# Kernel optimization log

Hardware: AMD Instinct MI355X
Metric: run time of the kernel (lower is better)

## Reference

```python
import jax, jax.numpy as jnp
import numpy as np

B_SI = 4.1491   # neutron scattering length Si (fm)
B_O = 5.803     # neutron scattering length O (fm)
CUTOFF = 3.5    # tetrahedral neighbour cutoff (A)
BIG = 1e6       # masked-distance sentinel (finite to keep grads NaN-free)


def setup_inputs() -> dict:
    key = jax.random.key(0)
    k1, k2 = jax.random.split(key)
    N, L = 4096, 40.0
    positions = jax.random.uniform(k1, (N, 3), dtype=jnp.float32) * L
    cell = (L * jnp.eye(3)).astype(jnp.float32)
    r_bins = (0.05 + 0.05 * jnp.arange(200, dtype=jnp.float32))      # 0.05..10.0 A
    q_bins = jnp.linspace(0.5, 25.0, 500, dtype=jnp.float32)          # A^-1
    species = jax.random.randint(k2, (N,), 0, 3, dtype=jnp.int32)     # 0=Si, 1/2=O
    return {"positions": positions, "cell": cell, "r_bins": r_bins,
            "q_bins": q_bins, "species": species}


def _pair_geometry(positions, cell):
    # Minimum-image displacements under a general periodic cell.
    disp = positions[:, None, :] - positions[None, :, :]        # [N,N,3]
    frac = disp @ jnp.linalg.inv(cell)
    frac = frac - jnp.round(frac)
    disp = frac @ cell
    d2 = jnp.sum(disp * disp, axis=-1)                           # [N,N]
    self_mask = jnp.eye(positions.shape[0], dtype=bool)
    dist = jnp.sqrt(jnp.where(self_mask, 1.0, d2))               # safe sqrt on diag
    return disp, dist, self_mask


def reference(positions, cell, r_bins, q_bins, species):
    N = positions.shape[0]
    nbins = r_bins.shape[0]
    dtype = positions.dtype

    disp, dist, self_mask = _pair_geometry(positions, cell)

    # --- neutron-weighted G(r): differentiable linear (cloud-in-cell) binning ---
    b = jnp.where(species == 0, B_SI, B_O).astype(dtype)         # per-atom scattering length
    w = (b[:, None] * b[None, :]) / (jnp.mean(b) ** 2)           # Faber-Ziman pair weights
    r0, dr = r_bins[0], r_bins[1] - r_bins[0]
    x = (dist - r0) / dr
    i0 = jnp.floor(x).astype(jnp.int32)
    f = x - i0.astype(dtype)
    valid = (~self_mask) & (i0 >= 0) & (i0 < nbins - 1)
    w0 = jnp.where(valid, w * (1.0 - f), 0.0).ravel()
    w1 = jnp.where(valid, w * f, 0.0).ravel()
    i0f = jnp.clip(i0, 0, nbins - 1).ravel()
    hist = (jnp.zeros(nbins, dtype)
            .at[i0f].add(w0)
            .at[jnp.clip(i0f + 1, 0, nbins - 1)].add(w1))
    V = jnp.abs(jnp.linalg.det(cell))
    rho = N / V
    shell = 4.0 * jnp.pi * r_bins ** 2 * dr                       # ideal-gas shell volume
    G_r = hist / (N * rho * shell)                                # [nbins]

    # --- total correlation function T(r) = 4 pi rho r G(r) ---
    T_r = 4.0 * jnp.pi * rho * r_bins * G_r

    # --- structure factor S(Q) = 1 + 4 pi rho int r^2 (G(r)-1) sinc(Qr) dr ---
    qr = q_bins[:, None] * r_bins[None, :]                        # [nQ, nr]
    integrand = (r_bins ** 2) * (G_r - 1.0)
    S_Q = 1.0 + 4.0 * jnp.pi * rho * dr * jnp.sum(
        integrand[None, :] * jnp.sinc(qr / jnp.pi), axis=1)

    # --- tetrahedral order parameter q_tet over Si centres with O neighbours ---
    central = species == 0
    nbr_ok = (species != 0)[None, :] & (~self_mask)
    nd = jnp.where(nbr_ok, dist, BIG)
    negd, idx = jax.lax.top_k(-nd, 4)                             # 4 nearest O per atom
    d4 = -negd                                                    # [N,4]
    u = jnp.take_along_axis(disp, idx[:, :, None], axis=1) / d4[:, :, None]  # unit vecs
    cosang = jnp.einsum('nkd,nld->nkl', u, u)                     # [N,4,4]
    pair_mask = jnp.triu(jnp.ones((4, 4), bool), 1)               # 6 angle pairs
    q_i = 1.0 - (3.0 / 8.0) * jnp.sum(((cosang + 1.0 / 3.0) ** 2) * pair_mask, axis=(1, 2))
    vf = (central & (d4[:, 3] < CUTOFF)).astype(dtype)            # needs 4 nbrs in cutoff
    q_tet = jnp.sum(q_i * vf) / jnp.maximum(jnp.sum(vf), 1.0)

    return G_r, T_r, S_Q, q_tet
```

## Files before the change

kernel.cpp:

```cpp
#include <hip/hip_runtime.h>
#include <climits>
#include <math.h>


#define B_SI_F 4.1491f
#define B_O_F  5.803f
#define CUTOFF_F 3.5f
#define CS2 12.25350025f
#define NCOPIES 16
#define CAP 32

#define WS_HIST 16
#define WS_ACC  3328
#define WS_CNT  4096

__device__ __forceinline__ bool dless(float da, int ia, float db, int ib) {
    return (da < db) || (da == db && ia < ib);
}

struct CellK {
    float ci0, ci1, ci2, ci3, ci4, ci5, ci6, ci7, ci8;
    float c0, c1, c2, c3, c4, c5, c6, c7, c8;
};

__device__ __forceinline__ CellK make_cell(const float* __restrict__ cellm,
                                           bool& diag) {
    CellK K;
    K.c0 = cellm[0]; K.c1 = cellm[1]; K.c2 = cellm[2];
    K.c3 = cellm[3]; K.c4 = cellm[4]; K.c5 = cellm[5];
    K.c6 = cellm[6]; K.c7 = cellm[7]; K.c8 = cellm[8];
    double m0 = K.c0, m1 = K.c1, m2 = K.c2;
    double m3 = K.c3, m4 = K.c4, m5 = K.c5;
    double m6 = K.c6, m7 = K.c7, m8 = K.c8;
    double det = m0*(m4*m8 - m5*m7) - m1*(m3*m8 - m5*m6) + m2*(m3*m7 - m4*m6);
    double rd = 1.0 / det;
    K.ci0 = (float)( (m4*m8 - m5*m7) * rd);
    K.ci1 = (float)(-(m1*m8 - m2*m7) * rd);
    K.ci2 = (float)( (m1*m5 - m2*m4) * rd);
    K.ci3 = (float)(-(m3*m8 - m5*m6) * rd);
    K.ci4 = (float)( (m0*m8 - m2*m6) * rd);
    K.ci5 = (float)(-(m0*m5 - m2*m3) * rd);
    K.ci6 = (float)( (m3*m7 - m4*m6) * rd);
    K.ci7 = (float)(-(m0*m7 - m1*m6) * rd);
    K.ci8 = (float)( (m0*m4 - m1*m3) * rd);
    diag = (K.c1 == 0.0f) && (K.c2 == 0.0f) && (K.c3 == 0.0f) &&
           (K.c5 == 0.0f) && (K.c6 == 0.0f) && (K.c7 == 0.0f);
    return K;
}

template<bool DIAG>
__device__ __forceinline__ void min_image(const CellK& K,
                                          float dx, float dy, float dz,
                                          float& ex, float& ey, float& ez) {
    if (DIAG) {
        float t0 = dx * K.ci0, t1 = dy * K.ci4, t2 = dz * K.ci8;
        t0 -= rintf(t0);  t1 -= rintf(t1);  t2 -= rintf(t2);
        ex = t0 * K.c0;  ey = t1 * K.c4;  ez = t2 * K.c8;
    } else {
        float f0 = dx*K.ci0 + dy*K.ci3 + dz*K.ci6;
        float f1 = dx*K.ci1 + dy*K.ci4 + dz*K.ci7;
        float f2 = dx*K.ci2 + dy*K.ci5 + dz*K.ci8;
        f0 -= rintf(f0);  f1 -= rintf(f1);  f2 -= rintf(f2);
        ex = f0*K.c0 + f1*K.c3 + f2*K.c6;
        ey = f0*K.c1 + f1*K.c4 + f2*K.c7;
        ez = f0*K.c2 + f1*K.c5 + f2*K.c8;
    }
}

template<bool DIAG>
__device__ __forceinline__ void hist_sweep(const CellK& K,
                                           const float4* __restrict__ sj,
                                           const float4* __restrict__ sjc,
                                           int lbase, int jb0,
                                           float fi0, float fi1, float fi2,
                                           float xi, float yi, float zi,
                                           float wi, float inv_dr, float nrb0,
                                           float dmax2, int nbins_m1,
                                           float* shist,
                                           bool iSi, bool iO, bool offdiag, int iidx,
                                           float* __restrict__ cnt,
                                           float4* __restrict__ cand) {
    #pragma unroll 4
    for (int l = 0; l < 32; ++l) {
        const float4 pj = sj[lbase + l];
        float d0 = fi0 - pj.x;  d0 -= rintf(d0);
        float d1 = fi1 - pj.y;  d1 -= rintf(d1);
        float d2 = fi2 - pj.z;  d2 -= rintf(d2);
        float ex, ey, ez;
        if (DIAG) {
            ex = d0 * K.c0;  ey = d1 * K.c4;  ez = d2 * K.c8;
        } else {
            ex = d0*K.c0 + d1*K.c3 + d2*K.c6;
            ey = d0*K.c1 + d1*K.c4 + d2*K.c7;
            ez = d0*K.c2 + d1*K.c5 + d2*K.c8;
        }
        float dsq = fmaf(ex, ex, fmaf(ey, ey, ez * ez));
        if (dsq < dmax2) {
            float dist = __builtin_amdgcn_sqrtf(dsq);
            float x  = fmaf(dist, inv_dr, nrb0);
            float fl = floorf(x);
            int   i0 = (int)fl;
            if ((unsigned)i0 < (unsigned)nbins_m1) {
                float w  = wi * pj.w;
                float wf = w * (x - fl);
                atomicAdd(&shist[i0],     w - wf);
                atomicAdd(&shist[i0 + 1], wf);
            }
            if (dsq < CS2) {
                const int jg = jb0 + lbase + l;
                if (iSi && pj.w == B_O_F) {
                    float old = atomicAdd(&cnt[iidx], 1.0f);
                    int slot = (int)rintf(old);
                    if (slot < CAP) {
                        float4 cj = sjc[lbase + l];
                        cj.w = __int_as_float(jg);
                        cand[iidx * CAP + slot] = cj;
                    }
                }
                if (offdiag && iO && pj.w == B_SI_F) {
                    float old = atomicAdd(&cnt[jg], 1.0f);
                    int slot = (int)rintf(old);
                    if (slot < CAP)
                        cand[jg * CAP + slot] = make_float4(xi, yi, zi, __int_as_float(iidx));
                }
            }
        }
    }
}

__global__ __launch_bounds__(256) void k_main(const float* __restrict__ cellm,
                                              const float* __restrict__ pos,
                                              const int* __restrict__ species,
                                              const float* __restrict__ rbins,
                                              float* __restrict__ ws,
                                              int N, int nbins, int T) {
    const int tid = threadIdx.x;
    const int bid = blockIdx.x;

    bool diag;
    const CellK K = make_cell(cellm, diag);

    __shared__ float shist[256];
    __shared__ float sjf[64 * 4];
    __shared__ float sjc[64 * 4];
    shist[tid] = 0.0f;

    const int jhalf = bid & 1;
    int rem = bid >> 1, ti = 0;
    while (rem >= T - ti) { rem -= T - ti; ti++; }
    const int tj  = ti + rem;
    const int jb0 = tj * 128 + jhalf * 64;

    if (tid < 192) {
        int g = 3 * jb0 + tid;
        sjc[(tid / 3) * 4 + (tid % 3)] = (g < 3 * N) ? pos[g] : 0.0f;
    } else {
        int a = tid - 192;
        int ja = jb0 + a;
        sjf[a * 4 + 3] = (ja < N) ? ((species[ja] == 0) ? B_SI_F : B_O_F) : 0.0f;
    }
    __syncthreads();
    if (tid < 64) {
        float x = sjc[tid*4], y = sjc[tid*4+1], z = sjc[tid*4+2];
        float f0, f1, f2;
        if (diag) { f0 = x*K.ci0; f1 = y*K.ci4; f2 = z*K.ci8; }
        else {
            f0 = x*K.ci0 + y*K.ci3 + z*K.ci6;
            f1 = x*K.ci1 + y*K.ci4 + z*K.ci7;
            f2 = x*K.ci2 + y*K.ci5 + z*K.ci8;
        }
        sjf[tid*4] = f0;  sjf[tid*4+1] = f1;  sjf[tid*4+2] = f2;
    }

    const float rb0      = rbins[0];
    const float dr       = rbins[1] - rbins[0];
    const float inv_dr   = 1.0f / dr;
    const float nrb0     = -rb0 * inv_dr;
    const int   nbins_m1 = nbins - 1;
    const float dmax     = fmaf((float)nbins_m1, dr, rb0);
    const float dmax2    = dmax * dmax * 1.000001f;

    const int il  = tid & 127;
    const int sub = tid >> 7;
    const int i   = ti * 128 + il;
    const int ig  = min(i, N - 1);
    const float xi = pos[3*ig], yi = pos[3*ig+1], zi = pos[3*ig+2];
    float fi0, fi1, fi2;
    if (diag) { fi0 = xi*K.ci0; fi1 = yi*K.ci4; fi2 = zi*K.ci8; }
    else {
        fi0 = xi*K.ci0 + yi*K.ci3 + zi*K.ci6;
        fi1 = xi*K.ci1 + yi*K.ci4 + zi*K.ci7;
        fi2 = xi*K.ci2 + yi*K.ci5 + zi*K.ci8;
    }
    const int   spi  = species[ig];
    const float b_i  = (spi == 0) ? B_SI_F : B_O_F;
    const float wmul = (ti == tj) ? 1.0f : 2.0f;
    const float wi   = (i < N) ? b_i * wmul : 0.0f;
    const bool iSi = (i < N) && (spi == 0);
    const bool iO  = (i < N) && (spi != 0);
    const bool offdiag = (ti != tj);

    float*  cnt  = ws + WS_CNT;
    float4* cand = (float4*)(ws + WS_CNT + (size_t)N);

    __syncthreads();

    const float4* sj   = (const float4*)sjf;
    const float4* sjc4 = (const float4*)sjc;
    const int lbase = sub * 32;
    if (diag) hist_sweep<true >(K, sj, sjc4, lbase, jb0, fi0, fi1, fi2, xi, yi, zi, wi, inv_dr, nrb0, dmax2, nbins_m1, shist, iSi, iO, offdiag, i, cnt, cand);
    else      hist_sweep<false>(K, sj, sjc4, lbase, jb0, fi0, fi1, fi2, xi, yi, zi, wi, inv_dr, nrb0, dmax2, nbins_m1, shist, iSi, iO, offdiag, i, cnt, cand);

    __syncthreads();

    float* gh = ws + WS_HIST + (size_t)(bid % NCOPIES) * nbins;
    for (int t = tid; t < nbins; t += 256) {
        float h = shist[t];
        if (h != 0.0f) atomicAdd(&gh[t], h);
    }
}

#define INS4D(c, jc, ex, ey, ez)                                           \
{                                                                          \
    if (dless(c, jc, e3, j3)) {                                            \
        bool lt2 = dless(c, jc, e2, j2);                                   \
        bool lt1 = dless(c, jc, e1, j1);                                   \
        bool lt0 = dless(c, jc, e0, j0);                                   \
        e3 = lt2 ? e2 : c;               j3 = lt2 ? j2 : jc;               \
        x3 = lt2 ? x2 : ex;  y3 = lt2 ? y2 : ey;  z3 = lt2 ? z2 : ez;      \
        e2 = lt2 ? (lt1 ? e1 : c) : e2;  j2 = lt2 ? (lt1 ? j1 : jc) : j2;  \
        x2 = lt2 ? (lt1 ? x1 : ex) : x2;                                   \
        y2 = lt2 ? (lt1 ? y1 : ey) : y2;                                   \
        z2 = lt2 ? (lt1 ? z1 : ez) : z2;                                   \
        e1 = lt1 ? (lt0 ? e0 : c) : e1;  j1 = lt1 ? (lt0 ? j0 : jc) : j1;  \
        x1 = lt1 ? (lt0 ? x0 : ex) : x1;                                   \
        y1 = lt1 ? (lt0 ? y0 : ey) : y1;                                   \
        z1 = lt1 ? (lt0 ? z0 : ez) : z1;                                   \
        e0 = lt0 ? c : e0;               j0 = lt0 ? jc : j0;               \
        x0 = lt0 ? ex : x0;  y0 = lt0 ? ey : y0;  z0 = lt0 ? ez : z0;      \
    }                                                                      \
}

__device__ __forceinline__ float fast_sinc(float x) {
    float rev = x * 0.15915494309189535f;
    rev -= rintf(rev);
    float sn = __builtin_amdgcn_sinf(rev);
    return sn * __builtin_amdgcn_rcpf(x);
}

__global__ __launch_bounds__(256) void k_fin(const float* __restrict__ cellm,
                                             float* __restrict__ ws,
                                             const float* __restrict__ rbins,
                                             const float* __restrict__ qbins,
                                             const int* __restrict__ species,
                                             const float* __restrict__ pos,
                                             float* __restrict__ out,
                                             int N, int nbins, int nq,
                                             int QB, int BT) {
    const int tid = threadIdx.x;
    const int bid = blockIdx.x;

    if (bid >= QB) {
        __shared__ float swq[4], swv[4];
        const int tb   = bid - QB;
        const int wid  = tid >> 6;
        const int lane = tid & 63;
        const int s = __builtin_amdgcn_readfirstlane(tb * 4 + wid);

        float* cnt = ws + WS_CNT;
        const float4* cand = (const float4*)(ws + WS_CNT + (size_t)N);

        float qiv = 0.0f, vf = 0.0f;
        if (s < N) {
            const int sp = species[s];
            const float xi = pos[3*s], yi = pos[3*s+1], zi = pos[3*s+2];
            const float cf = cnt[s];
            float4 cd = make_float4(0.f, 0.f, 0.f, 0.f);
            if (lane < CAP) cd = cand[(size_t)s * CAP + lane];
            bool diag;
            const CellK K = make_cell(cellm, diag);

            if (sp == 0) {
                if (lane == 0) cnt[s] = 0.0f;
                const int c = (int)rintf(cf);

                float e0 = 1e30f, e1 = 1e30f, e2 = 1e30f, e3 = 1e30f;
                int   j0 = INT_MAX, j1 = INT_MAX, j2 = INT_MAX, j3 = INT_MAX;
                float x0 = 0, y0 = 0, z0 = 0, x1 = 0, y1 = 0, z1 = 0;
                float x2 = 0, y2 = 0, z2 = 0, x3 = 0, y3 = 0, z3 = 0;

                if (c <= CAP) {
                    if (lane < c) {
                        int j = __float_as_int(cd.w);
                        float ex, ey, ez;
                        if (diag) min_image<true >(K, xi - cd.x, yi - cd.y, zi - cd.z, ex, ey, ez);
                        else      min_image<false>(K, xi - cd.x, yi - cd.y, zi - cd.z, ex, ey, ez);
                        e0 = fmaf(ex, ex, fmaf(ey, ey, ez * ez));
                        j0 = j;  x0 = ex;  y0 = ey;  z0 = ez;
                    }
                } else {
                    for (int k = lane; k < N; k += 64) {
                        int   spk = species[k];
                        float px = pos[3*k], py = pos[3*k+1], pz = pos[3*k+2];
                        float ex, ey, ez;
                        if (diag) min_image<true >(K, xi - px, yi - py, zi - pz, ex, ey, ez);
                        else      min_image<false>(K, xi - px, yi - py, zi - pz, ex, ey, ez);
                        float d2 = fmaf(ex, ex, fmaf(ey, ey, ez * ez));
                        float cc = (spk != 0 && k != s) ? d2 : 1e30f;
                        int   jc = k;
                        INS4D(cc, jc, ex, ey, ez)
                    }
                }

                float r0d, r1d, r2d, r3d;
                int   r0j, r1j, r2j, r3j;
                float rx[4], ry[4], rz[4];
                #define EXTRACT_MIN(RD, RJ, RK)                                    \
                {                                                                  \
                    float md = e0; int mj = j0;                                    \
                    float mx = x0, my = y0, mz = z0;                               \
                    for (int off = 32; off > 0; off >>= 1) {                       \
                        float od = __shfl_xor(md, off, 64);                        \
                        int   oj = __shfl_xor(mj, off, 64);                        \
                        float ox = __shfl_xor(mx, off, 64);                        \
                        float oy = __shfl_xor(my, off, 64);                        \
                        float oz = __shfl_xor(mz, off, 64);                        \
                        bool keep = dless(md, mj, od, oj);                         \
                        md = keep ? md : od;  mj = keep ? mj : oj;                 \
                        mx = keep ? mx : ox;  my = keep ? my : oy;                 \
                        mz = keep ? mz : oz;                                       \
                    }                                                              \
                    RD = md; RJ = mj; rx[RK] = mx; ry[RK] = my; rz[RK] = mz;       \
                    bool pop = (j0 == mj);                                         \
                    e0 = pop ? e1 : e0;  j0 = pop ? j1 : j0;                       \
                    x0 = pop ? x1 : x0;  y0 = pop ? y1 : y0;  z0 = pop ? z1 : z0;  \
                    e1 = pop ? e2 : e1;  j1 = pop ? j2 : j1;                       \
                    x1 = pop ? x2 : x1;  y1 = pop ? y2 : y1;  z1 = pop ? z2 : z1;  \
                    e2 = pop ? e3 : e2;  j2 = pop ? j3 : j2;                       \
                    x2 = pop ? x3 : x2;  y2 = pop ? y3 : y2;  z2 = pop ? z3 : z2;  \
                    e3 = pop ? 1e30f : e3;  j3 = pop ? INT_MAX : j3;               \
                }
                EXTRACT_MIN(r0d, r0j, 0)
                EXTRACT_MIN(r1d, r1j, 1)
                EXTRACT_MIN(r2d, r2j, 2)
                EXTRACT_MIN(r3d, r3j, 3)
                #undef EXTRACT_MIN

                if (lane == 0 && r3j != INT_MAX) {
                    float dd[4] = {sqrtf(r0d), sqrtf(r1d), sqrtf(r2d), sqrtf(r3d)};
                    if (dd[3] < CUTOFF_F) {
                        float ux[4], uy[4], uz[4];
                        #pragma unroll
                        for (int k = 0; k < 4; ++k) {
                            ux[k] = rx[k] / dd[k];
                            uy[k] = ry[k] / dd[k];
                            uz[k] = rz[k] / dd[k];
                        }
                        float s2 = 0.0f;
                        #pragma unroll
                        for (int k = 0; k < 4; ++k)
                            #pragma unroll
                            for (int l = k + 1; l < 4; ++l) {
                                float cs = ux[k]*ux[l] + uy[k]*uy[l] + uz[k]*uz[l];
                                float t  = cs + (1.0f / 3.0f);
                                s2 += t * t;
                            }
                        qiv = 1.0f - 0.375f * s2;
                        vf  = 1.0f;
                    }
                }
            }
        }
        if (lane == 0) { swq[wid] = qiv; swv[wid] = vf; }
        __syncthreads();
        if (tid == 0) {
            float bsq = swq[0] + swq[1] + swq[2] + swq[3];
            float bsv = swv[0] + swv[1] + swv[2] + swv[3];
            atomicAdd(&ws[WS_ACC + (tb & 63)], bsq);
            atomicAdd(&ws[WS_ACC + 64 + (tb & 63)], bsv);
        }
        return;
    }

    __shared__ float2 srw[256];
    __shared__ int    scnt[256];

    float hv[NCOPIES];
    const bool hb = (tid < nbins);
    if (hb) {
        #pragma unroll
        for (int c = 0; c < NCOPIES; ++c) hv[c] = ws[WS_HIST + c * nbins + tid];
    }

    double m0 = cellm[0], m1 = cellm[1], m2 = cellm[2];
    double m3 = cellm[3], m4 = cellm[4], m5 = cellm[5];
    double m6 = cellm[6], m7 = cellm[7], m8 = cellm[8];
    double det = m0*(m4*m8 - m5*m7) - m1*(m3*m8 - m5*m6) + m2*(m3*m7 - m4*m6);
    const float rho = (float)((double)N / fabs(det));

    {
        int c = 0;
        for (int k = tid; k < N; k += 256) c += (species[k] == 0) ? 1 : 0;
        scnt[tid] = c;
    }
    __syncthreads();
    for (int s = 128; s > 0; s >>= 1) {
        if (tid < s) scnt[tid] += scnt[tid + s];
        __syncthreads();
    }
    const int nSi = scnt[0];
    const float mean_b  = ((float)nSi * B_SI_F + (float)(N - nSi) * B_O_F) / (float)N;
    const float w_scale = 1.0f / (mean_b * mean_b);

    const float dr = rbins[1] - rbins[0];
    const float FOURPI = 4.0f * 3.14159265358979323846f;

    if (hb) {
        float h = 0.0f;
        #pragma unroll
        for (int c = 0; c < NCOPIES; ++c) h += hv[c];
        h *= w_scale;
        float r = rbins[tid];
        float shell = FOURPI * r * r * dr;
        float g = h / ((float)N * rho * shell);
        srw[tid] = make_float2(r, r * r * (g - 1.0f));
        if (bid == 0) {
            out[tid] = g;
            out[nbins + tid] = FOURPI * rho * r * g;
        }
    }
    __syncthreads();

    const int q = bid + QB * tid;
    if (q < nq) {
        float qq = qbins[q];
        float s0 = 0.0f, s1 = 0.0f, s2 = 0.0f, s3 = 0.0f;
        int t = 0;
        for (; t + 4 <= nbins; t += 4) {
            float2 a = srw[t], b = srw[t+1], c = srw[t+2], d = srw[t+3];
            s0 += a.y * fast_sinc(qq * a.x);
            s1 += b.y * fast_sinc(qq * b.x);
            s2 += c.y * fast_sinc(qq * c.x);
            s3 += d.y * fast_sinc(qq * d.x);
        }
        for (; t < nbins; ++t) {
            float2 a = srw[t];
            s0 += a.y * fast_sinc(qq * a.x);
        }
        float s = (s0 + s1) + (s2 + s3);
        out[2 * nbins + q] = 1.0f + FOURPI * rho * dr * s;
    }
}

__global__ __launch_bounds__(128) void k_qtet(const float* __restrict__ ws,
                                              float* __restrict__ out,
                                              int nbins, int nq) {
    __shared__ float sacc[128];
    const int tid = threadIdx.x;
    sacc[tid] = ws[WS_ACC + tid];
    __syncthreads();
    if (tid < 32) {
        float q = sacc[tid] + sacc[tid + 32];
        float v = sacc[64 + tid] + sacc[96 + tid];
        for (int off = 16; off > 0; off >>= 1) {
            q += __shfl_down(q, off, 64);
            v += __shfl_down(v, off, 64);
        }
        if (tid == 0)
            out[2 * nbins + nq] = q / fmaxf(v, 1.0f);
    }
}

extern "C" void kernel_launch(void* const* d_in, const int* in_sizes, int n_in,
                              void* d_out, int out_size, void* d_ws, size_t ws_size,
                              hipStream_t stream) {
    const float* pos     = (const float*)d_in[0];
    const float* cell    = (const float*)d_in[1];
    const float* rbins   = (const float*)d_in[2];
    const float* qbins   = (const float*)d_in[3];
    const int*   species = (const int*)d_in[4];
    float* out = (float*)d_out;
    float* ws  = (float*)d_ws;

    const int N     = in_sizes[4];
    const int nbins = in_sizes[2];
    const int nq    = in_sizes[3];

    const int T  = (N + 127) / 128;
    const int P2 = T * (T + 1);
    const int BT = (N + 3) / 4;
    const int QB = (nq + 63) / 64;

    k_main<<<P2, 256, 0, stream>>>(cell, pos, species, rbins, ws, N, nbins, T);
    k_fin<<<QB + BT, 256, 0, stream>>>(cell, ws, rbins, qbins, species, pos, out, N, nbins, nq, QB, BT);
    k_qtet<<<1, 128, 0, stream>>>(ws, out, nbins, nq);
}
```

Measured before the change: 88.19 us.

## Compact Si centres into a list and process four per wavefront in q_tet

The main kernel now appends Si atom indices to a compacted global list using a ballot plus an atomic counter. The q_tet phase in k_fin reads that list and gives each Si centre a 16-lane group instead of a whole 64-lane wavefront, so four centres share one wave and non-Si atoms no longer take up waves. Each lane handles two candidates and the top-4 extraction shuffles only within 16 lanes. The risks are the extra atomic and list writes in k_main, a list order that varies from run to run, and a launch that still allocates N/16 blocks, many of which find nothing to do.

```diff
diff --git a/kernel.cpp b/kernel.cpp
--- a/kernel.cpp
+++ b/kernel.cpp
@@ -12,6 +12,7 @@
 
 #define WS_HIST 16
 #define WS_ACC  3328
+#define WS_NSI  3456
 #define WS_CNT  4096
 
 __device__ __forceinline__ bool dless(float da, int ia, float db, int ib) {
@@ -202,6 +203,22 @@
 
     float*  cnt  = ws + WS_CNT;
     float4* cand = (float4*)(ws + WS_CNT + (size_t)N);
+    int*    silist = (int*)(ws + WS_CNT + (size_t)N + 4 * (size_t)N * CAP);
+
+    if (ti == tj && jhalf == 0 && tid < 128) {
+        const bool c_ = iSi;
+        unsigned long long m = __ballot(c_);
+        if (m != 0ULL) {
+            const int lane = tid & 63;
+            float base = 0.0f;
+            if (lane == 0) base = atomicAdd(&ws[WS_NSI], (float)__popcll(m));
+            base = __shfl(base, 0, 64);
+            if (c_) {
+                int rank = __popcll(m & ((1ULL << lane) - 1ULL));
+                silist[(int)rintf(base) + rank] = i;
+            }
+        }
+    }
 
     __syncthreads();
 
@@ -256,7 +273,7 @@
                                              const float* __restrict__ pos,
                                              float* __restrict__ out,
                                              int N, int nbins, int nq,
-                                             int QB, int BT) {
+                                             int QB, int BTT) {
     const int tid = threadIdx.x;
     const int bid = blockIdx.x;
 
@@ -265,112 +282,128 @@
         const int tb   = bid - QB;
         const int wid  = tid >> 6;
         const int lane = tid & 63;
-        const int s = __builtin_amdgcn_readfirstlane(tb * 4 + wid);
+        const int ga   = lane >> 4;
+        const int gl   = lane & 15;
+        const int g    = tb * 16 + wid * 4 + ga;
 
         float* cnt = ws + WS_CNT;
         const float4* cand = (const float4*)(ws + WS_CNT + (size_t)N);
+        const int* silist  = (const int*)(ws + WS_CNT + (size_t)N + 4 * (size_t)N * CAP);
+
+        const int nsi = (int)rintf(ws[WS_NSI]);
+        int s = -1;
+        if (g < nsi) s = silist[g];
 
         float qiv = 0.0f, vf = 0.0f;
-        if (s < N) {
-            const int sp = species[s];
+        if (s >= 0) {
             const float xi = pos[3*s], yi = pos[3*s+1], zi = pos[3*s+2];
             const float cf = cnt[s];
-            float4 cd = make_float4(0.f, 0.f, 0.f, 0.f);
-            if (lane < CAP) cd = cand[(size_t)s * CAP + lane];
+            const float4 cd0 = cand[(size_t)s * CAP + gl];
+            const float4 cd1 = cand[(size_t)s * CAP + gl + 16];
             bool diag;
             const CellK K = make_cell(cellm, diag);
 
-            if (sp == 0) {
-                if (lane == 0) cnt[s] = 0.0f;
-                const int c = (int)rintf(cf);
-
-                float e0 = 1e30f, e1 = 1e30f, e2 = 1e30f, e3 = 1e30f;
-                int   j0 = INT_MAX, j1 = INT_MAX, j2 = INT_MAX, j3 = INT_MAX;
-                float x0 = 0, y0 = 0, z0 = 0, x1 = 0, y1 = 0, z1 = 0;
-                float x2 = 0, y2 = 0, z2 = 0, x3 = 0, y3 = 0, z3 = 0;
-
-                if (c <= CAP) {
-                    if (lane < c) {
-                        int j = __float_as_int(cd.w);
-                        float ex, ey, ez;
-                        if (diag) min_image<true >(K, xi - cd.x, yi - cd.y, zi - cd.z, ex, ey, ez);
-                        else      min_image<false>(K, xi - cd.x, yi - cd.y, zi - cd.z, ex, ey, ez);
-                        e0 = fmaf(ex, ex, fmaf(ey, ey, ez * ez));
-                        j0 = j;  x0 = ex;  y0 = ey;  z0 = ez;
-                    }
-                } else {
-                    for (int k = lane; k < N; k += 64) {
-                        int   spk = species[k];
-                        float px = pos[3*k], py = pos[3*k+1], pz = pos[3*k+2];
-                        float ex, ey, ez;
-                        if (diag) min_image<true >(K, xi - px, yi - py, zi - pz, ex, ey, ez);
-                        else      min_image<false>(K, xi - px, yi - py, zi - pz, ex, ey, ez);
-                        float d2 = fmaf(ex, ex, fmaf(ey, ey, ez * ez));
-                        float cc = (spk != 0 && k != s) ? d2 : 1e30f;
-                        int   jc = k;
-                        INS4D(cc, jc, ex, ey, ez)
-                    }
+            if (gl == 0) cnt[s] = 0.0f;
+            const int c = (int)rintf(cf);
+
+            float e0 = 1e30f, e1 = 1e30f, e2 = 1e30f, e3 = 1e30f;
+            int   j0 = INT_MAX, j1 = INT_MAX, j2 = INT_MAX, j3 = INT_MAX;
+            float x0 = 0, y0 = 0, z0 = 0, x1 = 0, y1 = 0, z1 = 0;
+            float x2 = 0, y2 = 0, z2 = 0, x3 = 0, y3 = 0, z3 = 0;
+
+            if (c <= CAP) {
+                if (gl < c) {
+                    int j = __float_as_int(cd0.w);
+                    float ex, ey, ez;
+                    if (diag) min_image<true >(K, xi - cd0.x, yi - cd0.y, zi - cd0.z, ex, ey, ez);
+                    else      min_image<false>(K, xi - cd0.x, yi - cd0.y, zi - cd0.z, ex, ey, ez);
+                    float d2v = fmaf(ex, ex, fmaf(ey, ey, ez * ez));
+                    INS4D(d2v, j, ex, ey, ez)
                 }
-
-                float r0d, r1d, r2d, r3d;
-                int   r0j, r1j, r2j, r3j;
-                float rx[4], ry[4], rz[4];
-                #define EXTRACT_MIN(RD, RJ, RK)                                    \
-                {                                                                  \
-                    float md = e0; int mj = j0;                                    \
-                    float mx = x0, my = y0, mz = z0;                               \
-                    for (int off = 32; off > 0; off >>= 1) {                       \
-                        float od = __shfl_xor(md, off, 64);                        \
-                        int   oj = __shfl_xor(mj, off, 64);                        \
-                        float ox = __shfl_xor(mx, off, 64);                        \
-                        float oy = __shfl_xor(my, off, 64);                        \
-                        float oz = __shfl_xor(mz, off, 64);                        \
-                        bool keep = dless(md, mj, od, oj);                         \
-                        md = keep ? md : od;  mj = keep ? mj : oj;                 \
-                        mx = keep ? mx : ox;  my = keep ? my : oy;                 \
-                        mz = keep ? mz : oz;                                       \
-                    }                                                              \
-                    RD = md; RJ = mj; rx[RK] = mx; ry[RK] = my; rz[RK] = mz;       \
-                    bool pop = (j0 == mj);                                         \
-                    e0 = pop ? e1 : e0;  j0 = pop ? j1 : j0;                       \
-                    x0 = pop ? x1 : x0;  y0 = pop ? y1 : y0;  z0 = pop ? z1 : z0;  \
-                    e1 = pop ? e2 : e1;  j1 = pop ? j2 : j1;                       \
-                    x1 = pop ? x2 : x1;  y1 = pop ? y2 : y1;  z1 = pop ? z2 : z1;  \
-                    e2 = pop ? e3 : e2;  j2 = pop ? j3 : j2;                       \
-                    x2 = pop ? x3 : x2;  y2 = pop ? y3 : y2;  z2 = pop ? z3 : z2;  \
-                    e3 = pop ? 1e30f : e3;  j3 = pop ? INT_MAX : j3;               \
+                if (gl + 16 < c) {
+                    int j = __float_as_int(cd1.w);
+                    float ex, ey, ez;
+                    if (diag) min_image<true >(K, xi - cd1.x, yi - cd1.y, zi - cd1.z, ex, ey, ez);
+                    else      min_image<false>(K, xi - cd1.x, yi - cd1.y, zi - cd1.z, ex, ey, ez);
+                    float d2v = fmaf(ex, ex, fmaf(ey, ey, ez * ez));
+                    INS4D(d2v, j, ex, ey, ez)
                 }
-                EXTRACT_MIN(r0d, r0j, 0)
-                EXTRACT_MIN(r1d, r1j, 1)
-                EXTRACT_MIN(r2d, r2j, 2)
-                EXTRACT_MIN(r3d, r3j, 3)
-                #undef EXTRACT_MIN
-
-                if (lane == 0 && r3j != INT_MAX) {
-                    float dd[4] = {sqrtf(r0d), sqrtf(r1d), sqrtf(r2d), sqrtf(r3d)};
-                    if (dd[3] < CUTOFF_F) {
-                        float ux[4], uy[4], uz[4];
-                        #pragma unroll
-                        for (int k = 0; k < 4; ++k) {
-                            ux[k] = rx[k] / dd[k];
-                            uy[k] = ry[k] / dd[k];
-                            uz[k] = rz[k] / dd[k];
-                        }
-                        float s2 = 0.0f;
-                        #pragma unroll
-                        for (int k = 0; k < 4; ++k)
-                            #pragma unroll
-                            for (int l = k + 1; l < 4; ++l) {
-                                float cs = ux[k]*ux[l] + uy[k]*uy[l] + uz[k]*uz[l];
-                                float t  = cs + (1.0f / 3.0f);
-                                s2 += t * t;
-                            }
-                        qiv = 1.0f - 0.375f * s2;
-                        vf  = 1.0f;
-                    }
+            } else {
+                for (int k = gl; k < N; k += 16) {
+                    int   spk = species[k];
+                    float px = pos[3*k], py = pos[3*k+1], pz = pos[3*k+2];
+                    float ex, ey, ez;
+                    if (diag) min_image<true >(K, xi - px, yi - py, zi - pz, ex, ey, ez);
+                    else      min_image<false>(K, xi - px, yi - py, zi - pz, ex, ey, ez);
+                    float d2v = fmaf(ex, ex, fmaf(ey, ey, ez * ez));
+                    float cc = (spk != 0 && k != s) ? d2v : 1e30f;
+                    int   jc = k;
+                    INS4D(cc, jc, ex, ey, ez)
                 }
             }
-        }
+
+            float r0d, r1d, r2d, r3d;
+            int   r0j, r1j, r2j, r3j;
+            float rx[4], ry[4], rz[4];
+            #define EXTRACT_MIN16(RD, RJ, RK)                                  \
+            {                                                                  \
+                float md = e0; int mj = j0;                                    \
+                float mx = x0, my = y0, mz = z0;                               \
+                for (int off = 8; off > 0; off >>= 1) {                        \
+                    float od = __shfl_xor(md, off, 64);                        \
+                    int   oj = __shfl_xor(mj, off, 64);                        \
+                    float ox = __shfl_xor(mx, off, 64);                        \
+                    float oy = __shfl_xor(my, off, 64);                        \
+                    float oz = __shfl_xor(mz, off, 64);                        \
+                    bool keep = dless(md, mj, od, oj);                         \
+                    md = keep ? md : od;  mj = keep ? mj : oj;                 \
+                    mx = keep ? mx : ox;  my = keep ? my : oy;                 \
+                    mz = keep ? mz : oz;                                       \
+                }                                                              \
+                RD = md; RJ = mj; rx[RK] = mx; ry[RK] = my; rz[RK] = mz;       \
+                bool pop = (j0 == mj);                                         \
+                e0 = pop ? e1 : e0;  j0 = pop ? j1 : j0;                       \
+                x0 = pop ? x1 : x0;  y0 = pop ? y1 : y0;  z0 = pop ? z1 : z0;  \
+                e1 = pop ? e2 : e1;  j1 = pop ? j2 : j1;                       \
+                x1 = pop ? x2 : x1;  y1 = pop ? y2 : y1;  z1 = pop ? z2 : z1;  \
+                e2 = pop ? e3 : e2;  j2 = pop ? j3 : j2;                       \
+                x2 = pop ? x3 : x2;  y2 = pop ? y3 : y2;  z2 = pop ? z3 : z2;  \
+                e3 = pop ? 1e30f : e3;  j3 = pop ? INT_MAX : j3;               \
+            }
+            EXTRACT_MIN16(r0d, r0j, 0)
+            EXTRACT_MIN16(r1d, r1j, 1)
+            EXTRACT_MIN16(r2d, r2j, 2)
+            EXTRACT_MIN16(r3d, r3j, 3)
+            #undef EXTRACT_MIN16
+
+            if (gl == 0 && r3j != INT_MAX) {
+                float dd[4] = {sqrtf(r0d), sqrtf(r1d), sqrtf(r2d), sqrtf(r3d)};
+                if (dd[3] < CUTOFF_F) {
+                    float ux[4], uy[4], uz[4];
+                    #pragma unroll
+                    for (int k = 0; k < 4; ++k) {
+                        ux[k] = rx[k] / dd[k];
+                        uy[k] = ry[k] / dd[k];
+                        uz[k] = rz[k] / dd[k];
+                    }
+                    float s2 = 0.0f;
+                    #pragma unroll
+                    for (int k = 0; k < 4; ++k)
+                        #pragma unroll
+                        for (int l = k + 1; l < 4; ++l) {
+                            float cs = ux[k]*ux[l] + uy[k]*uy[l] + uz[k]*uz[l];
+                            float t  = cs + (1.0f / 3.0f);
+                            s2 += t * t;
+                        }
+                    qiv = 1.0f - 0.375f * s2;
+                    vf  = 1.0f;
+                }
+            }
+        }
+        qiv += __shfl_xor(qiv, 16, 64);
+        qiv += __shfl_xor(qiv, 32, 64);
+        vf  += __shfl_xor(vf, 16, 64);
+        vf  += __shfl_xor(vf, 32, 64);
         if (lane == 0) { swq[wid] = qiv; swv[wid] = vf; }
         __syncthreads();
         if (tid == 0) {
@@ -452,12 +485,13 @@
     }
 }
 
-__global__ __launch_bounds__(128) void k_qtet(const float* __restrict__ ws,
+__global__ __launch_bounds__(128) void k_qtet(float* __restrict__ ws,
                                               float* __restrict__ out,
                                               int nbins, int nq) {
     __shared__ float sacc[128];
     const int tid = threadIdx.x;
     sacc[tid] = ws[WS_ACC + tid];
+    if (tid == 0) ws[WS_NSI] = 0.0f;
     __syncthreads();
     if (tid < 32) {
         float q = sacc[tid] + sacc[tid + 32];
@@ -486,12 +520,12 @@
     const int nbins = in_sizes[2];
     const int nq    = in_sizes[3];
 
-    const int T  = (N + 127) / 128;
-    const int P2 = T * (T + 1);
-    const int BT = (N + 3) / 4;
-    const int QB = (nq + 63) / 64;
+    const int T   = (N + 127) / 128;
+    const int P2  = T * (T + 1);
+    const int BTT = (N + 15) / 16;
+    const int QB  = (nq + 63) / 64;
 
     k_main<<<P2, 256, 0, stream>>>(cell, pos, species, rbins, ws, N, nbins, T);
-    k_fin<<<QB + BT, 256, 0, stream>>>(cell, ws, rbins, qbins, species, pos, out, N, nbins, nq, QB, BT);
+    k_fin<<<QB + BTT, 256, 0, stream>>>(cell, ws, rbins, qbins, species, pos, out, N, nbins, nq, QB, BTT);
     k_qtet<<<1, 128, 0, stream>>>(ws, out, nbins, nq);
 }
```

After: 87.17 us. About the same (-1.2%).
